# Performance work log

Measured on AMD Instinct MI355X. Metric: run time of the kernel, lower is better.

## Reference

```python
import jax, jax.numpy as jnp
import numpy as np

B, D, H, O, E = 4096, 1024, 4096, 1024, 8
TOP_K = 2


def setup_inputs() -> dict:
    key = jax.random.key(0)
    ks = jax.random.split(key, 7)
    s = 0.02
    return {
        "expert_input": jax.random.normal(ks[0], (B, D), dtype=jnp.float32),
        "Wg": jax.random.normal(ks[1], (D, E), dtype=jnp.float32) * s,
        "bg": jnp.zeros((E,), dtype=jnp.float32),
        "W1": jax.random.normal(ks[2], (E, D, H), dtype=jnp.float32) * s,
        "b1": jnp.zeros((E, H), dtype=jnp.float32),
        "W2": jax.random.normal(ks[3], (E, H, O), dtype=jnp.float32) * s,
        "b2": jnp.zeros((E, O), dtype=jnp.float32),
    }


def reference(expert_input, Wg, bg, W1, b1, W2, b2):
    x = expert_input                                  # [B, D]
    gate_logits = x @ Wg + bg                         # [B, E]
    topk_logits, topk_idx = jax.lax.top_k(gate_logits, TOP_K)
    topk_w = jax.nn.softmax(topk_logits, axis=1)      # softmax over the k selected logits
    rows = jnp.arange(x.shape[0])[:, None]
    dense_w = jnp.zeros_like(gate_logits).at[rows, topk_idx].set(topk_w)  # [B, E]
    # Dense (all-experts) evaluation; zero gate weight == unrouted, so math
    # matches the masked per-expert loop in the torch module exactly.
    h = jax.nn.relu(jnp.einsum('bd,edh->ebh', x, W1) + b1[:, None, :])    # [E, B, H]
    expert_out = jnp.einsum('ebh,eho->ebo', h, W2) + b2[:, None, :]       # [E, B, O]
    routed = jnp.einsum('be,ebo->bo', dense_w, expert_out)                # [B, O]
    return routed
```

## Files before the change

kernel.cpp:

```cpp
#include <hip/hip_runtime.h>
#include <cstdint>

#define DEVI __device__ __forceinline__

typedef __bf16 bf16x8_t __attribute__((ext_vector_type(8)));
typedef float f32x4_t __attribute__((ext_vector_type(4)));

typedef const __attribute__((address_space(1))) unsigned int* gas_t;
typedef __attribute__((address_space(3))) unsigned int* las_t;

DEVI void glds16(const void* g, void* l) {
  __builtin_amdgcn_global_load_lds((gas_t)g, (las_t)l, 16, 0, 0);
}

DEVI uint16_t f2b(float f) {
  uint32_t u = __builtin_bit_cast(uint32_t, f);
  u += 0x7fffu + ((u >> 16) & 1u);
  return (uint16_t)(u >> 16);
}

static constexpr int MAXT = 72;

__global__ __launch_bounds__(256) void moe_gate(const float* __restrict__ x,
    const float* __restrict__ Wg, const float* __restrict__ bg,
    int* __restrict__ gidx, float* __restrict__ gw, uint16_t* __restrict__ xb) {
  const int lane = threadIdx.x & 63;
  const int b = blockIdx.x * 4 + (threadIdx.x >> 6);
  float acc[8];
#pragma unroll
  for (int e = 0; e < 8; ++e) acc[e] = 0.f;
  const float* xr = x + (size_t)b * 1024;
  uint16_t* xbr = xb + (size_t)b * 1024;
#pragma unroll
  for (int it = 0; it < 4; ++it) {
    const int d0 = it * 256 + lane * 4;
    float4 xv = *(const float4*)(xr + d0);
    uint64_t pk = (uint64_t)f2b(xv.x) | ((uint64_t)f2b(xv.y) << 16) |
                  ((uint64_t)f2b(xv.z) << 32) | ((uint64_t)f2b(xv.w) << 48);
    *(uint64_t*)(xbr + d0) = pk;
    float xs[4] = {xv.x, xv.y, xv.z, xv.w};
#pragma unroll
    for (int q = 0; q < 4; ++q) {
      const float4* wrow = (const float4*)(Wg + (size_t)(d0 + q) * 8);
      float4 wa = wrow[0], wb = wrow[1];
      acc[0] += xs[q] * wa.x; acc[1] += xs[q] * wa.y;
      acc[2] += xs[q] * wa.z; acc[3] += xs[q] * wa.w;
      acc[4] += xs[q] * wb.x; acc[5] += xs[q] * wb.y;
      acc[6] += xs[q] * wb.z; acc[7] += xs[q] * wb.w;
    }
  }
#pragma unroll
  for (int off = 32; off; off >>= 1)
#pragma unroll
    for (int e = 0; e < 8; ++e) acc[e] += __shfl_xor(acc[e], off, 64);
  if (lane == 0) {
    float l[8];
#pragma unroll
    for (int e = 0; e < 8; ++e) l[e] = acc[e] + bg[e];
    int i0 = 0;
#pragma unroll
    for (int e = 1; e < 8; ++e) if (l[e] > l[i0]) i0 = e;
    int i1 = (i0 == 0) ? 1 : 0;
#pragma unroll
    for (int e = 0; e < 8; ++e) if (e != i0 && l[e] > l[i1]) i1 = e;
    float ex = expf(l[i1] - l[i0]);
    float s = 1.f + ex;
    gidx[2 * b] = i0; gidx[2 * b + 1] = i1;
    gw[2 * b] = 1.f / s; gw[2 * b + 1] = ex / s;
  }
}

__global__ __launch_bounds__(256) void moe_scan(const int* __restrict__ gidx,
                                                int* __restrict__ meta) {
  __shared__ int cnt[8];
  if (threadIdx.x < 8) cnt[threadIdx.x] = 0;
  __syncthreads();
  int loc[8] = {0, 0, 0, 0, 0, 0, 0, 0};
  for (int i = threadIdx.x; i < 8192; i += 256) {
    int e = gidx[i];
#pragma unroll
    for (int q = 0; q < 8; ++q) loc[q] += (e == q) ? 1 : 0;
  }
#pragma unroll
  for (int q = 0; q < 8; ++q) atomicAdd(&cnt[q], loc[q]);
  __syncthreads();
  if (threadIdx.x == 0) {
    int off = 0, t = 0;
    for (int e = 0; e < 8; ++e) {
      int c = cnt[e];
      meta[e] = c;
      meta[8 + e] = off;
      meta[17 + e] = 0;
      int nt = (c + 127) >> 7;
      for (int mt = 0; mt < nt; ++mt) {
        meta[32 + t] = e;
        meta[104 + t] = off + mt * 128;
        meta[176 + t] = off + c;
        ++t;
      }
      off += c;
    }
    meta[16] = off;
    meta[25] = t;
  }
}

__global__ __launch_bounds__(256) void moe_scatter(const int* __restrict__ gidx,
    const float* __restrict__ gw, int* __restrict__ meta,
    int* __restrict__ row_index, float* __restrict__ row_w) {
  int i = blockIdx.x * 256 + threadIdx.x;
  int e = gidx[i];
  int pos = meta[8 + e] + atomicAdd(&meta[17 + e], 1);
  row_index[pos] = i >> 1;
  row_w[pos] = gw[i];
}

__global__ __launch_bounds__(256) void moe_transpose(const float* __restrict__ in,
                                                     uint16_t* __restrict__ outp,
                                                     int K, int N) {
  __shared__ uint16_t t[64][72];
  const int e = blockIdx.z;
  const int k0 = blockIdx.y * 64, n0 = blockIdx.x * 64;
  const int r = threadIdx.x >> 2;
  const int c0 = (threadIdx.x & 3) * 16;
  const float* src = in + ((size_t)e * K + k0 + r) * N + n0 + c0;
#pragma unroll
  for (int q = 0; q < 4; ++q) {
    float4 v = *(const float4*)(src + q * 4);
    uint64_t pk = (uint64_t)f2b(v.x) | ((uint64_t)f2b(v.y) << 16) |
                  ((uint64_t)f2b(v.z) << 32) | ((uint64_t)f2b(v.w) << 48);
    *(uint64_t*)&t[r][c0 + q * 4] = pk;
  }
  __syncthreads();
  alignas(16) uint16_t buf[16];
#pragma unroll
  for (int j = 0; j < 16; ++j) buf[j] = t[c0 + j][r];
  uint16_t* dst = outp + ((size_t)e * N + n0 + r) * K + k0 + c0;
  *(uint4*)dst = *(const uint4*)&buf[0];
  *(uint4*)(dst + 8) = *(const uint4*)&buf[8];
}

template <int KD, int ND, int MODE, int KSL>
__global__ __launch_bounds__(256, 4) void moe_gemm(
    const uint16_t* __restrict__ Am, const uint16_t* __restrict__ Bt,
    const float* __restrict__ bias, const int* __restrict__ meta,
    const int* __restrict__ row_index, const float* __restrict__ row_w,
    uint16_t* __restrict__ hout, float* __restrict__ out) {
  constexpr int NB = ND / 128;
  constexpr int KSLEN = KD / KSL;
  constexpr int NIT = KSLEN / 32;
  const int nwg = gridDim.x;
  const int orig = blockIdx.x;
  const int q8 = nwg >> 3, r8 = nwg & 7, xcd = orig & 7, loc = orig >> 3;
  int wg = (xcd < r8 ? xcd * (q8 + 1) : r8 * (q8 + 1) + (xcd - r8) * q8) + loc;
  const int nb = wg % NB; wg /= NB;
  const int ks = wg % KSL; wg /= KSL;
  const int ty = wg;
  if (ty >= meta[25]) return;
  const int e = meta[32 + ty];
  const int pos0 = meta[104 + ty];
  const int vend = meta[176 + ty];
  const int k0 = ks * KSLEN;

  __shared__ uint16_t As[2][128 * 32];
  __shared__ uint16_t Bs[2][128 * 32];

  const int tid = threadIdx.x;
  const int lane = tid & 63;
  const int w = tid >> 6;
  const int wr = w >> 1, wc = w & 1;

  size_t aoff[2], boff[2];
#pragma unroll
  for (int j = 0; j < 2; ++j) {
    int c = j * 256 + tid;
    int row = c >> 2;
    int skc = (c & 3) ^ ((row >> 1) & 3);
    int pos = pos0 + row;
    if (pos > 8191) pos = 8191;
    int ar = (MODE == 1) ? row_index[pos] : pos;
    aoff[j] = ((size_t)ar * KD + (size_t)k0 + (size_t)skc * 8) * 2;
    boff[j] = (((size_t)e * ND + (size_t)nb * 128 + row) * KD + (size_t)k0 + (size_t)skc * 8) * 2;
  }
  const char* Ag = (const char*)Am;
  const char* Bg = (const char*)Bt;

  f32x4_t acc[4][4];
  f32x4_t z;
  z[0] = 0.f; z[1] = 0.f; z[2] = 0.f; z[3] = 0.f;
#pragma unroll
  for (int m = 0; m < 4; ++m)
#pragma unroll
    for (int n = 0; n < 4; ++n) acc[m][n] = z;

  auto stage = [&](int buf, int t) {
#pragma unroll
    for (int j = 0; j < 2; ++j) {
      glds16(Ag + aoff[j] + (size_t)t * 64, &As[buf][(j * 256 + w * 64) * 8]);
      glds16(Bg + boff[j] + (size_t)t * 64, &Bs[buf][(j * 256 + w * 64) * 8]);
    }
  };

  stage(0, 0);
  __syncthreads();
  int cur = 0;
  for (int t = 0; t < NIT; ++t) {
    if (t + 1 < NIT) stage(cur ^ 1, t + 1);
    const uint16_t* Ap = As[cur];
    const uint16_t* Bp = Bs[cur];
    bf16x8_t af[4], bfr[4];
#pragma unroll
    for (int m = 0; m < 4; ++m) {
      int row = wr * 64 + m * 16 + (lane & 15);
      int skc = ((lane >> 4) ^ (row >> 1)) & 3;
      af[m] = *(const bf16x8_t*)(Ap + row * 32 + skc * 8);
    }
#pragma unroll
    for (int n = 0; n < 4; ++n) {
      int row = wc * 64 + n * 16 + (lane & 15);
      int skc = ((lane >> 4) ^ (row >> 1)) & 3;
      bfr[n] = *(const bf16x8_t*)(Bp + row * 32 + skc * 8);
    }
#pragma unroll
    for (int m = 0; m < 4; ++m)
#pragma unroll
      for (int n = 0; n < 4; ++n)
        acc[m][n] = __builtin_amdgcn_mfma_f32_16x16x32_bf16(af[m], bfr[n], acc[m][n], 0, 0, 0);
    __syncthreads();
    cur ^= 1;
  }

  const int cb = nb * 128 + wc * 64;
  if constexpr (MODE == 1) {
#pragma unroll
    for (int m = 0; m < 4; ++m) {
      int pr = pos0 + wr * 64 + m * 16 + ((lane >> 4) << 2);
#pragma unroll
      for (int i = 0; i < 4; ++i) {
        int pos = pr + i;
        if (pos < vend) {
#pragma unroll
          for (int n = 0; n < 4; ++n) {
            int col = cb + n * 16 + (lane & 15);
            float v = acc[m][n][i] + bias[e * ND + col];
            v = fmaxf(v, 0.f);
            hout[(size_t)pos * ND + col] = f2b(v);
          }
        }
      }
    }
  } else {
#pragma unroll
    for (int m = 0; m < 4; ++m) {
      int pr = pos0 + wr * 64 + m * 16 + ((lane >> 4) << 2);
#pragma unroll
      for (int i = 0; i < 4; ++i) {
        int pos = pr + i;
        if (pos < vend) {
          int bi = row_index[pos];
          float wgt = row_w[pos];
          float* orow = out + (size_t)bi * ND;
#pragma unroll
          for (int n = 0; n < 4; ++n) {
            int col = cb + n * 16 + (lane & 15);
            float bterm = (ks == 0) ? bias[e * ND + col] : 0.f;
            atomicAdd(orow + col, (acc[m][n][i] + bterm) * wgt);
          }
        }
      }
    }
  }
}

extern "C" void kernel_launch(void* const* d_in, const int* in_sizes, int n_in,
                              void* d_out, int out_size, void* d_ws, size_t ws_size,
                              hipStream_t stream) {
  const float* x  = (const float*)d_in[0];
  const float* Wg = (const float*)d_in[1];
  const float* bg = (const float*)d_in[2];
  const float* W1 = (const float*)d_in[3];
  const float* b1 = (const float*)d_in[4];
  const float* W2 = (const float*)d_in[5];
  const float* b2 = (const float*)d_in[6];
  float* out = (float*)d_out;

  char* ws = (char*)d_ws;
  uint16_t* w1t = (uint16_t*)ws; ws += (size_t)8 * 4096 * 1024 * 2;
  uint16_t* w2t = (uint16_t*)ws; ws += (size_t)8 * 1024 * 4096 * 2;
  uint16_t* xb  = (uint16_t*)ws; ws += (size_t)4096 * 1024 * 2;
  uint16_t* h   = (uint16_t*)ws; ws += (size_t)8192 * 4096 * 2;
  int*   gidx = (int*)ws;   ws += 8192 * 4;
  float* gw   = (float*)ws; ws += 8192 * 4;
  int*   rix  = (int*)ws;   ws += 8192 * 4;
  float* rw   = (float*)ws; ws += 8192 * 4;
  int*   meta = (int*)ws;   ws += 4096;

  hipMemsetAsync(d_out, 0, (size_t)4096 * 1024 * 4, stream);
  moe_gate<<<1024, 256, 0, stream>>>(x, Wg, bg, gidx, gw, xb);
  moe_transpose<<<dim3(4096 / 64, 1024 / 64, 8), 256, 0, stream>>>(W1, w1t, 1024, 4096);
  moe_transpose<<<dim3(1024 / 64, 4096 / 64, 8), 256, 0, stream>>>(W2, w2t, 4096, 1024);
  moe_scan<<<1, 256, 0, stream>>>(gidx, meta);
  moe_scatter<<<32, 256, 0, stream>>>(gidx, gw, meta, rix, rw);
  moe_gemm<1024, 4096, 1, 1><<<dim3(32 * MAXT), 256, 0, stream>>>(
      xb, w1t, b1, meta, rix, rw, h, nullptr);
  moe_gemm<4096, 1024, 2, 2><<<dim3(8 * 2 * MAXT), 256, 0, stream>>>(
      h, w2t, b2, meta, rix, rw, nullptr, out);
}
```

Measured before the change: 477.8 us.

## Rewrite MoE GEMM main loop with manual waitcnt pipelining and drop split-K

```diff
diff --git a/kernel.cpp b/kernel.cpp
--- a/kernel.cpp
+++ b/kernel.cpp
@@ -17,6 +17,20 @@
   uint32_t u = __builtin_bit_cast(uint32_t, f);
   u += 0x7fffu + ((u >> 16) & 1u);
   return (uint16_t)(u >> 16);
+}
+
+template <int IMM>
+DEVI f32x4_t ldsr(uint32_t addr) {
+  f32x4_t r;
+  if constexpr (IMM == 0)
+    asm volatile("ds_read_b128 %0, %1" : "=v"(r) : "v"(addr));
+  else if constexpr (IMM == 1024)
+    asm volatile("ds_read_b128 %0, %1 offset:1024" : "=v"(r) : "v"(addr));
+  else if constexpr (IMM == 2048)
+    asm volatile("ds_read_b128 %0, %1 offset:2048" : "=v"(r) : "v"(addr));
+  else
+    asm volatile("ds_read_b128 %0, %1 offset:3072" : "=v"(r) : "v"(addr));
+  return r;
 }
 
 static constexpr int MAXT = 72;
@@ -140,30 +154,26 @@
   *(uint4*)(dst + 8) = *(const uint4*)&buf[8];
 }
 
-template <int KD, int ND, int MODE, int KSL>
-__global__ __launch_bounds__(256, 4) void moe_gemm(
+template <int KD, int ND, int MODE>
+__global__ __launch_bounds__(256, 5) void moe_gemm(
     const uint16_t* __restrict__ Am, const uint16_t* __restrict__ Bt,
     const float* __restrict__ bias, const int* __restrict__ meta,
     const int* __restrict__ row_index, const float* __restrict__ row_w,
     uint16_t* __restrict__ hout, float* __restrict__ out) {
   constexpr int NB = ND / 128;
-  constexpr int KSLEN = KD / KSL;
-  constexpr int NIT = KSLEN / 32;
+  constexpr int NIT = KD / 32;
+  __shared__ uint16_t sm[4][128 * 32];
+
   const int nwg = gridDim.x;
   const int orig = blockIdx.x;
   const int q8 = nwg >> 3, r8 = nwg & 7, xcd = orig & 7, loc = orig >> 3;
   int wg = (xcd < r8 ? xcd * (q8 + 1) : r8 * (q8 + 1) + (xcd - r8) * q8) + loc;
-  const int nb = wg % NB; wg /= NB;
-  const int ks = wg % KSL; wg /= KSL;
-  const int ty = wg;
+  const int nb = wg % NB;
+  const int ty = wg / NB;
   if (ty >= meta[25]) return;
   const int e = meta[32 + ty];
   const int pos0 = meta[104 + ty];
   const int vend = meta[176 + ty];
-  const int k0 = ks * KSLEN;
-
-  __shared__ uint16_t As[2][128 * 32];
-  __shared__ uint16_t Bs[2][128 * 32];
 
   const int tid = threadIdx.x;
   const int lane = tid & 63;
@@ -179,11 +189,19 @@
     int pos = pos0 + row;
     if (pos > 8191) pos = 8191;
     int ar = (MODE == 1) ? row_index[pos] : pos;
-    aoff[j] = ((size_t)ar * KD + (size_t)k0 + (size_t)skc * 8) * 2;
-    boff[j] = (((size_t)e * ND + (size_t)nb * 128 + row) * KD + (size_t)k0 + (size_t)skc * 8) * 2;
+    aoff[j] = ((size_t)ar * KD + (size_t)skc * 8) * 2;
+    boff[j] = (((size_t)e * ND + (size_t)nb * 128 + row) * KD + (size_t)skc * 8) * 2;
   }
   const char* Ag = (const char*)Am;
   const char* Bg = (const char*)Bt;
+
+  auto stage = [&](int s, int kt) {
+#pragma unroll
+    for (int j = 0; j < 2; ++j) {
+      glds16(Ag + aoff[j] + (size_t)kt * 64, &sm[s][(j * 256 + w * 64) * 8]);
+      glds16(Bg + boff[j] + (size_t)kt * 64, &sm[2 + s][(j * 256 + w * 64) * 8]);
+    }
+  };
 
   f32x4_t acc[4][4];
   f32x4_t z;
@@ -193,42 +211,40 @@
 #pragma unroll
     for (int n = 0; n < 4; ++n) acc[m][n] = z;
 
-  auto stage = [&](int buf, int t) {
-#pragma unroll
-    for (int j = 0; j < 2; ++j) {
-      glds16(Ag + aoff[j] + (size_t)t * 64, &As[buf][(j * 256 + w * 64) * 8]);
-      glds16(Bg + boff[j] + (size_t)t * 64, &Bs[buf][(j * 256 + w * 64) * 8]);
-    }
-  };
+  const uint32_t skcf = (uint32_t)(((lane >> 4) ^ ((lane & 15) >> 1)) & 3);
+  const uint32_t base = (uint32_t)(size_t)&sm[0][0];
+  const uint32_t aB0 = base + (uint32_t)((wr * 64 + (lane & 15)) * 64) + skcf * 16;
+  const uint32_t bB0 = base + 16384 + (uint32_t)((wc * 64 + (lane & 15)) * 64) + skcf * 16;
 
   stage(0, 0);
-  __syncthreads();
-  int cur = 0;
   for (int t = 0; t < NIT; ++t) {
-    if (t + 1 < NIT) stage(cur ^ 1, t + 1);
-    const uint16_t* Ap = As[cur];
-    const uint16_t* Bp = Bs[cur];
-    bf16x8_t af[4], bfr[4];
-#pragma unroll
-    for (int m = 0; m < 4; ++m) {
-      int row = wr * 64 + m * 16 + (lane & 15);
-      int skc = ((lane >> 4) ^ (row >> 1)) & 3;
-      af[m] = *(const bf16x8_t*)(Ap + row * 32 + skc * 8);
-    }
-#pragma unroll
-    for (int n = 0; n < 4; ++n) {
-      int row = wc * 64 + n * 16 + (lane & 15);
-      int skc = ((lane >> 4) ^ (row >> 1)) & 3;
-      bfr[n] = *(const bf16x8_t*)(Bp + row * 32 + skc * 8);
-    }
+    int tc = t + 1; if (tc > NIT - 1) tc = NIT - 1;
+    stage((t + 1) & 1, tc);
+    asm volatile("s_waitcnt vmcnt(4)" ::: "memory");
+    __builtin_amdgcn_s_barrier();
+
+    const uint32_t aA = aB0 + (uint32_t)((t & 1) * 8192);
+    const uint32_t bA = bB0 + (uint32_t)((t & 1) * 8192);
+    f32x4_t av[4], bv[4];
+    av[0] = ldsr<0>(aA); av[1] = ldsr<1024>(aA);
+    av[2] = ldsr<2048>(aA); av[3] = ldsr<3072>(aA);
+    bv[0] = ldsr<0>(bA); bv[1] = ldsr<1024>(bA);
+    bv[2] = ldsr<2048>(bA); bv[3] = ldsr<3072>(bA);
+    asm volatile("s_waitcnt lgkmcnt(0)" ::: "memory");
+    __builtin_amdgcn_sched_barrier(0);
+
+    __builtin_amdgcn_s_setprio(1);
 #pragma unroll
     for (int m = 0; m < 4; ++m)
 #pragma unroll
       for (int n = 0; n < 4; ++n)
-        acc[m][n] = __builtin_amdgcn_mfma_f32_16x16x32_bf16(af[m], bfr[n], acc[m][n], 0, 0, 0);
-    __syncthreads();
-    cur ^= 1;
-  }
+        acc[m][n] = __builtin_amdgcn_mfma_f32_16x16x32_bf16(
+            __builtin_bit_cast(bf16x8_t, av[m]), __builtin_bit_cast(bf16x8_t, bv[n]),
+            acc[m][n], 0, 0, 0);
+    __builtin_amdgcn_s_setprio(0);
+    __builtin_amdgcn_s_barrier();
+  }
+  asm volatile("s_waitcnt vmcnt(0)" ::: "memory");
 
   const int cb = nb * 128 + wc * 64;
   if constexpr (MODE == 1) {
@@ -263,8 +279,8 @@
 #pragma unroll
           for (int n = 0; n < 4; ++n) {
             int col = cb + n * 16 + (lane & 15);
-            float bterm = (ks == 0) ? bias[e * ND + col] : 0.f;
-            atomicAdd(orow + col, (acc[m][n][i] + bterm) * wgt);
+            float v = (acc[m][n][i] + bias[e * ND + col]) * wgt;
+            atomicAdd(orow + col, v);
           }
         }
       }
@@ -301,8 +317,8 @@
   moe_transpose<<<dim3(1024 / 64, 4096 / 64, 8), 256, 0, stream>>>(W2, w2t, 4096, 1024);
   moe_scan<<<1, 256, 0, stream>>>(gidx, meta);
   moe_scatter<<<32, 256, 0, stream>>>(gidx, gw, meta, rix, rw);
-  moe_gemm<1024, 4096, 1, 1><<<dim3(32 * MAXT), 256, 0, stream>>>(
+  moe_gemm<1024, 4096, 1><<<dim3(32 * MAXT), 256, 0, stream>>>(
       xb, w1t, b1, meta, rix, rw, h, nullptr);
-  moe_gemm<4096, 1024, 2, 2><<<dim3(8 * 2 * MAXT), 256, 0, stream>>>(
+  moe_gemm<4096, 1024, 2><<<dim3(8 * MAXT), 256, 0, stream>>>(
       h, w2t, b2, meta, rix, rw, nullptr, out);
 }
```

New measurement: 976.5 us. +104.4%, slower.
